# Kernel optimization log

Measured on AMD Instinct MI355X. Metric: run time of the kernel, lower is better.

## Reference

```python
import jax, jax.numpy as jnp
import numpy as np

BATCH, DIM = 8192, 1024  # batch of ODE states, state dimension (orig dim=100 scaled up)
ETA = 1.0                # self.eta
B_DECAY = 1.0            # self.B (linear decay coefficient)


def setup_inputs() -> dict:
    key = jax.random.key(0)
    k1, k2, k3, k4, k5 = jax.random.split(key, 5)
    return {
        "x":      jax.random.normal(k1, (BATCH, DIM), jnp.float32),
        "e_x":    jax.random.normal(k2, (BATCH, DIM), jnp.float32),
        "W":      jax.random.normal(k3, (BATCH, DIM), jnp.float32),
        "A":      jax.random.normal(k4, (DIM, DIM), jnpp := jnp.float32) / np.float32(np.sqrt(DIM)),
        "target": jax.random.normal(k5, (1, DIM), jnp.float32),
    }


def reference(x, e_x, W, A, target):
    # b_ast = diagonal of B_ast = diag(target^2 / (1 + target^2)); mm with a diag
    # matrix == elementwise multiply by its diagonal.  [1, D]
    b_ast = target ** 2 / (1.0 + target ** 2)
    # control: u = -eta * (W * (x + e_x - target)) @ B_ast              [B, D]
    u = -ETA * (W * ((x + e_x) - target)) * b_ast
    # saturating nonlinearity sigma(x) = x^2 / (1 + x^2)                [B, D]
    sig = x ** 2 / (1.0 + x ** 2)
    # dx = -B*x + A @ sigma(x) (per state: sigma(x) @ A^T) + u*sigma(x) [B, D]
    dx = -B_DECAY * x + sig @ A.T + u * sig
    # original returns tuple(dx_i) + tuple(-dx_i) + tuple(zeros): stack as [3, B, D]
    return jnp.stack([dx, -dx, jnp.zeros_like(dx)])
```

## Files before the change

kernel.cpp:

```cpp
#include <hip/hip_runtime.h>
#include <hip/hip_bf16.h>
#include <stdint.h>

#define BATCH 8192
#define DIM   1024
#define BM 128
#define BN 64
#define BK 64
#define STEPS 16
#define BUF 24576

typedef __attribute__((ext_vector_type(4))) float f32x4;
typedef __attribute__((ext_vector_type(8))) short bf16x8;
typedef __attribute__((ext_vector_type(8))) unsigned short u16x8;

#define AS1(p) ((const __attribute__((address_space(1))) void*)(p))
#define AS3(p) ((__attribute__((address_space(3))) void*)(p))

__device__ __forceinline__ unsigned short f2bf(float f) {
    union { __hip_bfloat16 h; unsigned short u; } v;
    v.h = __hip_bfloat16(f);
    return v.u;
}
__device__ __forceinline__ float sigma_f(float x) {
    float x2 = x * x;
    return x2 * __builtin_amdgcn_rcpf(1.0f + x2);
}

__global__ __launch_bounds__(256) void prep_kernel(
    const float* __restrict__ x, const float* __restrict__ A,
    unsigned short* __restrict__ sigb, unsigned short* __restrict__ Abf,
    float* __restrict__ out2)
{
    const int i = blockIdx.x * 256 + threadIdx.x;
    if (i < BATCH * DIM / 8) {
        f32x4 v0 = ((const f32x4*)x)[i * 2];
        f32x4 v1 = ((const f32x4*)x)[i * 2 + 1];
        u16x8 sb;
#pragma unroll
        for (int e = 0; e < 4; ++e) {
            sb[e]     = f2bf(sigma_f(v0[e]));
            sb[e + 4] = f2bf(sigma_f(v1[e]));
        }
        ((u16x8*)sigb)[i] = sb;
        ((f32x4*)out2)[i * 2]     = f32x4{0.f, 0.f, 0.f, 0.f};
        ((f32x4*)out2)[i * 2 + 1] = f32x4{0.f, 0.f, 0.f, 0.f};
    } else {
        const int j = i - BATCH * DIM / 8;
        f32x4 v0 = ((const f32x4*)A)[j * 2];
        f32x4 v1 = ((const f32x4*)A)[j * 2 + 1];
        u16x8 ab;
#pragma unroll
        for (int e = 0; e < 4; ++e) {
            ab[e]     = f2bf(v0[e]);
            ab[e + 4] = f2bf(v1[e]);
        }
        ((u16x8*)Abf)[j] = ab;
    }
}

__global__ __launch_bounds__(512, 4) void gemm_kernel(
    const float* __restrict__ x, const float* __restrict__ ex,
    const float* __restrict__ W, const float* __restrict__ tgt,
    const unsigned short* __restrict__ sigb,
    const unsigned short* __restrict__ Abf,
    float* __restrict__ out0, float* __restrict__ out1)
{
    __shared__ __align__(16) char lds[3 * BUF];

    const int b     = blockIdx.x;
    const int xcd   = b & 7;
    const int local = b >> 3;
    const int bm    = xcd * 8 + (local >> 4);
    const int bn    = local & 15;

    const int tid  = threadIdx.x;
    const int lane = tid & 63;
    const int wid  = tid >> 6;
    const int wr   = wid >> 1, wc = wid & 1;
    const int l15  = lane & 15;

    const int swz = (((lane & 7) ^ (lane >> 3)) << 4);
    const char* gS = (const char*)sigb +
        ((size_t)(bm * BM + wid * 8 + (lane >> 3)) * DIM) * 2 + swz;
    const char* gB = (const char*)Abf +
        ((size_t)(bn * BN + wid * 8 + (lane >> 3)) * DIM) * 2 + swz;

    const int rd_sw = (lane & 7) << 4;
    const int cb0   = (lane >> 4) << 4;

    f32x4 acc[2][2];
#pragma unroll
    for (int mi = 0; mi < 2; ++mi)
#pragma unroll
        for (int ni = 0; ni < 2; ++ni)
            acc[mi][ni] = f32x4{0.f, 0.f, 0.f, 0.f};

    auto stage = [&](int t) {
        char* As = lds + (t % 3) * BUF;
        char* Bs = As + 16384;
        const size_t ko = (size_t)t * (BK * 2);
#pragma unroll
        for (int j = 0; j < 2; ++j)
            __builtin_amdgcn_global_load_lds(
                AS1(gS + (size_t)j * (64 * DIM * 2) + ko),
                AS3(As + (wid * 8 + j * 64) * 128), 16, 0, 0);
        __builtin_amdgcn_global_load_lds(
            AS1(gB + ko), AS3(Bs + wid * 8 * 128), 16, 0, 0);
    };

    stage(0);
    stage(1);

    for (int t = 0; t < STEPS; ++t) {
        __builtin_amdgcn_sched_barrier(0);
        if (t < STEPS - 1) asm volatile("s_waitcnt vmcnt(3)" ::: "memory");
        else               asm volatile("s_waitcnt vmcnt(0)" ::: "memory");
        __builtin_amdgcn_sched_barrier(0);
        __builtin_amdgcn_s_barrier();
        __builtin_amdgcn_sched_barrier(0);
        if (t + 2 < STEPS) stage(t + 2);
        __builtin_amdgcn_sched_barrier(0);

        const char* As_ = lds + (t % 3) * BUF;
        const char* Bs_ = As_ + 16384;
#pragma unroll
        for (int kk = 0; kk < 2; ++kk) {
            bf16x8 af[2], bfr[2];
#pragma unroll
            for (int mi = 0; mi < 2; ++mi)
                af[mi] = *(const bf16x8*)(As_ + (wr * 32 + mi * 16 + l15) * 128 +
                                          ((cb0 + kk * 64) ^ rd_sw));
#pragma unroll
            for (int ni = 0; ni < 2; ++ni)
                bfr[ni] = *(const bf16x8*)(Bs_ + (wc * 32 + ni * 16 + l15) * 128 +
                                           ((cb0 + kk * 64) ^ rd_sw));
#pragma unroll
            for (int mi = 0; mi < 2; ++mi)
#pragma unroll
                for (int ni = 0; ni < 2; ++ni)
                    acc[mi][ni] = __builtin_amdgcn_mfma_f32_16x16x32_bf16(
                        af[mi], bfr[ni], acc[mi][ni], 0, 0, 0);
        }
    }

    __syncthreads();
#pragma unroll
    for (int mi = 0; mi < 2; ++mi)
#pragma unroll
        for (int ni = 0; ni < 2; ++ni) {
            const int row_ = wr * 32 + mi * 16 + ((lane >> 4) << 2);
            const int colb = (wc * 32 + ni * 16 + l15) * 4;
#pragma unroll
            for (int r = 0; r < 4; ++r)
                *(float*)(lds + (row_ + r) * 256 + colb) = acc[mi][ni][r];
        }
    __syncthreads();

#pragma unroll
    for (int p = 0; p < 4; ++p) {
        const int ci  = p * 512 + tid;
        const int row = ci >> 4;
        const int cv  = ci & 15;
        f32x4 c = *(const f32x4*)(lds + row * 256 + cv * 16);
        const size_t v4 = (size_t)(bm * BM + row) * (DIM / 4) + bn * 16 + cv;
        f32x4 xv = ((const f32x4*)x)[v4];
        f32x4 ev = ((const f32x4*)ex)[v4];
        f32x4 wv = ((const f32x4*)W)[v4];
        f32x4 tv = ((const f32x4*)tgt)[bn * 16 + cv];
        f32x4 o0;
#pragma unroll
        for (int e = 0; e < 4; ++e) {
            float xi = xv[e], ti = tv[e];
            float ba = ti * ti * __builtin_amdgcn_rcpf(1.0f + ti * ti);
            float u  = -(wv[e] * (xi + ev[e] - ti)) * ba;
            float s  = sigma_f(xi);
            o0[e] = -xi + u * s + c[e];
        }
        ((f32x4*)out0)[v4] = o0;
        ((f32x4*)out1)[v4] = -o0;
    }
}

extern "C" void kernel_launch(void* const* d_in, const int* in_sizes, int n_in,
                              void* d_out, int out_size, void* d_ws, size_t ws_size,
                              hipStream_t stream)
{
    const float* x   = (const float*)d_in[0];
    const float* ex  = (const float*)d_in[1];
    const float* W   = (const float*)d_in[2];
    const float* A   = (const float*)d_in[3];
    const float* tgt = (const float*)d_in[4];

    float* out0 = (float*)d_out;
    float* out1 = out0 + (size_t)BATCH * DIM;
    float* out2 = out1 + (size_t)BATCH * DIM;

    unsigned short* sigb = (unsigned short*)d_ws;
    unsigned short* Abf  = (unsigned short*)((char*)d_ws + (size_t)16 * 1024 * 1024);

    prep_kernel<<<4608, 256, 0, stream>>>(x, A, sigb, Abf, out2);
    gemm_kernel<<<(BATCH / BM) * (DIM / BN), 512, 0, stream>>>(
        x, ex, W, tgt, sigb, Abf, out0, out1);
}
```

Before: 57.34 us.

## Process two N tiles per block and overlap epilogue with next tile's GEMM

```diff
diff --git a/kernel.cpp b/kernel.cpp
--- a/kernel.cpp
+++ b/kernel.cpp
@@ -7,7 +7,6 @@
 #define BM 128
 #define BN 64
 #define BK 64
-#define STEPS 16
 #define BUF 24576
 
 typedef __attribute__((ext_vector_type(4))) float f32x4;
@@ -71,58 +70,121 @@
     const int b     = blockIdx.x;
     const int xcd   = b & 7;
     const int local = b >> 3;
-    const int bm    = xcd * 8 + (local >> 4);
-    const int bn    = local & 15;
+    const int bm    = xcd * 8 + (local >> 3);
+    const int bn0   = local & 7;
+    const int bn1   = bn0 + 8;
 
     const int tid  = threadIdx.x;
     const int lane = tid & 63;
     const int wid  = tid >> 6;
     const int wr   = wid >> 1, wc = wid & 1;
     const int l15  = lane & 15;
+    const int l4   = lane >> 4;
 
     const int swz = (((lane & 7) ^ (lane >> 3)) << 4);
     const char* gS = (const char*)sigb +
         ((size_t)(bm * BM + wid * 8 + (lane >> 3)) * DIM) * 2 + swz;
-    const char* gB = (const char*)Abf +
-        ((size_t)(bn * BN + wid * 8 + (lane >> 3)) * DIM) * 2 + swz;
+    const char* gB0 = (const char*)Abf +
+        ((size_t)(bn0 * BN + wid * 8 + (lane >> 3)) * DIM) * 2 + swz;
+    const char* gB1 = (const char*)Abf +
+        ((size_t)(bn1 * BN + wid * 8 + (lane >> 3)) * DIM) * 2 + swz;
 
     const int rd_sw = (lane & 7) << 4;
-    const int cb0   = (lane >> 4) << 4;
-
-    f32x4 acc[2][2];
+    const int cb0   = l4 << 4;
+
+    f32x4 acc0[2][2], acc1[2][2];
 #pragma unroll
     for (int mi = 0; mi < 2; ++mi)
 #pragma unroll
-        for (int ni = 0; ni < 2; ++ni)
-            acc[mi][ni] = f32x4{0.f, 0.f, 0.f, 0.f};
-
-    auto stage = [&](int t) {
-        char* As = lds + (t % 3) * BUF;
+        for (int ni = 0; ni < 2; ++ni) {
+            acc0[mi][ni] = f32x4{0.f, 0.f, 0.f, 0.f};
+            acc1[mi][ni] = f32x4{0.f, 0.f, 0.f, 0.f};
+        }
+
+    auto evi = [&](int bn, int mi, int ni) -> size_t {
+        return (size_t)(bm * BM + wr * 32 + mi * 16 + l15) * (DIM / 4)
+               + bn * 16 + wc * 8 + ni * 4 + l4;
+    };
+
+    f32x4 eX[2][2], eE[2][2], eW[2][2], tv[2];
+
+#pragma unroll
+    for (int ni = 0; ni < 2; ++ni)
+        tv[ni] = ((const f32x4*)tgt)[bn0 * 16 + wc * 8 + ni * 4 + l4];
+
+    auto stage = [&](int s) {
+        char* As = lds + (s % 3) * BUF;
         char* Bs = As + 16384;
-        const size_t ko = (size_t)t * (BK * 2);
+        const char* gb = (s < 16) ? gB0 : gB1;
+        const size_t ko = (size_t)((s < 16) ? s : s - 16) * (BK * 2);
 #pragma unroll
         for (int j = 0; j < 2; ++j)
             __builtin_amdgcn_global_load_lds(
                 AS1(gS + (size_t)j * (64 * DIM * 2) + ko),
                 AS3(As + (wid * 8 + j * 64) * 128), 16, 0, 0);
         __builtin_amdgcn_global_load_lds(
-            AS1(gB + ko), AS3(Bs + wid * 8 * 128), 16, 0, 0);
+            AS1(gb + ko), AS3(Bs + wid * 8 * 128), 16, 0, 0);
+    };
+
+    auto epiLoad = [&](int bn) {
+#pragma unroll
+        for (int mi = 0; mi < 2; ++mi)
+#pragma unroll
+            for (int ni = 0; ni < 2; ++ni) {
+                const size_t v4 = evi(bn, mi, ni);
+                eX[mi][ni] = ((const f32x4*)x)[v4];
+                eE[mi][ni] = ((const f32x4*)ex)[v4];
+                eW[mi][ni] = ((const f32x4*)W)[v4];
+            }
+    };
+
+    auto epiStore = [&](int bn, f32x4 (&acc)[2][2]) {
+#pragma unroll
+        for (int mi = 0; mi < 2; ++mi)
+#pragma unroll
+            for (int ni = 0; ni < 2; ++ni) {
+                const size_t v4 = evi(bn, mi, ni);
+                f32x4 o0;
+#pragma unroll
+                for (int e = 0; e < 4; ++e) {
+                    float xi = eX[mi][ni][e], ti = tv[ni][e];
+                    float ba = ti * ti * __builtin_amdgcn_rcpf(1.0f + ti * ti);
+                    float u  = -(eW[mi][ni][e] * (xi + eE[mi][ni][e] - ti)) * ba;
+                    float sg = sigma_f(xi);
+                    o0[e] = -xi + u * sg + acc[mi][ni][e];
+                }
+                ((f32x4*)out0)[v4] = o0;
+                ((f32x4*)out1)[v4] = -o0;
+            }
     };
 
     stage(0);
     stage(1);
 
-    for (int t = 0; t < STEPS; ++t) {
-        __builtin_amdgcn_sched_barrier(0);
-        if (t < STEPS - 1) asm volatile("s_waitcnt vmcnt(3)" ::: "memory");
-        else               asm volatile("s_waitcnt vmcnt(0)" ::: "memory");
+#pragma unroll
+    for (int s = 0; s < 32; ++s) {
+        __builtin_amdgcn_sched_barrier(0);
+        if (s == 9 || s == 10)       asm volatile("s_waitcnt vmcnt(15)" ::: "memory");
+        else if (s == 17 || s == 18) asm volatile("s_waitcnt vmcnt(11)" ::: "memory");
+        else if (s == 25 || s == 26) asm volatile("s_waitcnt vmcnt(17)" ::: "memory");
+        else if (s == 31)            asm volatile("s_waitcnt vmcnt(0)"  ::: "memory");
+        else                         asm volatile("s_waitcnt vmcnt(3)"  ::: "memory");
         __builtin_amdgcn_sched_barrier(0);
         __builtin_amdgcn_s_barrier();
         __builtin_amdgcn_sched_barrier(0);
-        if (t + 2 < STEPS) stage(t + 2);
-        __builtin_amdgcn_sched_barrier(0);
-
-        const char* As_ = lds + (t % 3) * BUF;
+        if (s + 2 < 32) stage(s + 2);
+        __builtin_amdgcn_sched_barrier(0);
+        if (s == 8) epiLoad(bn0);
+        if (s == 24) {
+#pragma unroll
+            for (int ni = 0; ni < 2; ++ni)
+                tv[ni] = ((const f32x4*)tgt)[bn1 * 16 + wc * 8 + ni * 4 + l4];
+            epiLoad(bn1);
+        }
+        if (s == 16) epiStore(bn0, acc0);
+        __builtin_amdgcn_sched_barrier(0);
+
+        const char* As_ = lds + (s % 3) * BUF;
         const char* Bs_ = As_ + 16384;
 #pragma unroll
         for (int kk = 0; kk < 2; ++kk) {
@@ -135,51 +197,25 @@
             for (int ni = 0; ni < 2; ++ni)
                 bfr[ni] = *(const bf16x8*)(Bs_ + (wc * 32 + ni * 16 + l15) * 128 +
                                            ((cb0 + kk * 64) ^ rd_sw));
-#pragma unroll
-            for (int mi = 0; mi < 2; ++mi)
-#pragma unroll
-                for (int ni = 0; ni < 2; ++ni)
-                    acc[mi][ni] = __builtin_amdgcn_mfma_f32_16x16x32_bf16(
-                        af[mi], bfr[ni], acc[mi][ni], 0, 0, 0);
+            if (s < 16) {
+#pragma unroll
+                for (int mi = 0; mi < 2; ++mi)
+#pragma unroll
+                    for (int ni = 0; ni < 2; ++ni)
+                        acc0[mi][ni] = __builtin_amdgcn_mfma_f32_16x16x32_bf16(
+                            bfr[ni], af[mi], acc0[mi][ni], 0, 0, 0);
+            } else {
+#pragma unroll
+                for (int mi = 0; mi < 2; ++mi)
+#pragma unroll
+                    for (int ni = 0; ni < 2; ++ni)
+                        acc1[mi][ni] = __builtin_amdgcn_mfma_f32_16x16x32_bf16(
+                            bfr[ni], af[mi], acc1[mi][ni], 0, 0, 0);
+            }
         }
     }
 
-    __syncthreads();
-#pragma unroll
-    for (int mi = 0; mi < 2; ++mi)
-#pragma unroll
-        for (int ni = 0; ni < 2; ++ni) {
-            const int row_ = wr * 32 + mi * 16 + ((lane >> 4) << 2);
-            const int colb = (wc * 32 + ni * 16 + l15) * 4;
-#pragma unroll
-            for (int r = 0; r < 4; ++r)
-                *(float*)(lds + (row_ + r) * 256 + colb) = acc[mi][ni][r];
-        }
-    __syncthreads();
-
-#pragma unroll
-    for (int p = 0; p < 4; ++p) {
-        const int ci  = p * 512 + tid;
-        const int row = ci >> 4;
-        const int cv  = ci & 15;
-        f32x4 c = *(const f32x4*)(lds + row * 256 + cv * 16);
-        const size_t v4 = (size_t)(bm * BM + row) * (DIM / 4) + bn * 16 + cv;
-        f32x4 xv = ((const f32x4*)x)[v4];
-        f32x4 ev = ((const f32x4*)ex)[v4];
-        f32x4 wv = ((const f32x4*)W)[v4];
-        f32x4 tv = ((const f32x4*)tgt)[bn * 16 + cv];
-        f32x4 o0;
-#pragma unroll
-        for (int e = 0; e < 4; ++e) {
-            float xi = xv[e], ti = tv[e];
-            float ba = ti * ti * __builtin_amdgcn_rcpf(1.0f + ti * ti);
-            float u  = -(wv[e] * (xi + ev[e] - ti)) * ba;
-            float s  = sigma_f(xi);
-            o0[e] = -xi + u * s + c[e];
-        }
-        ((f32x4*)out0)[v4] = o0;
-        ((f32x4*)out1)[v4] = -o0;
-    }
+    epiStore(bn1, acc1);
 }
 
 extern "C" void kernel_launch(void* const* d_in, const int* in_sizes, int n_in,
@@ -200,6 +236,5 @@
     unsigned short* Abf  = (unsigned short*)((char*)d_ws + (size_t)16 * 1024 * 1024);
 
     prep_kernel<<<4608, 256, 0, stream>>>(x, A, sigb, Abf, out2);
-    gemm_kernel<<<(BATCH / BM) * (DIM / BN), 512, 0, stream>>>(
-        x, ex, W, tgt, sigb, Abf, out0, out1);
-}
+    gemm_kernel<<<512, 512, 0, stream>>>(x, ex, W, tgt, sigb, Abf, out0, out1);
+}
```

Result: slower. 88.05 us (+53.5%).
